# Kernel optimization log

Measured on AMD Instinct MI355X. Metric: run time of the kernel, lower is better.

## Reference

```python
import jax, jax.numpy as jnp
import numpy as np

EPS = 1e-5
POOL = 4  # two stacked AvgPool3d(2) == one AvgPool3d(4, stride=4) on the valid region


def setup_inputs() -> dict:
    key = jax.random.key(0)
    k1, k2, k3 = jax.random.split(key, 3)
    N, Cin, Cout, D = 16, 32, 16, 32
    x = jax.random.normal(k1, (N, Cin, D, D, D), dtype=jnp.float32)
    w = jax.random.normal(k2, (Cin, Cout, 3, 3, 3), dtype=jnp.float32) * 0.1
    b = jax.random.normal(k3, (Cout,), dtype=jnp.float32) * 0.1
    gamma = jnp.ones((Cout,), dtype=jnp.float32)
    beta = jnp.zeros((Cout,), dtype=jnp.float32)
    return {"x": x, "w": w, "b": b, "gamma": gamma, "beta": beta}


def _convT_bn_pool(x, w, b, gamma, beta):
    # ConvTranspose3d(stride=2, padding=1, K=3) == dilated conv with
    # lhs_dilation=2, padding=K-1-p=1, spatially-flipped kernel, IO->OI swap.
    wt = jnp.flip(w, axis=(2, 3, 4)).transpose(1, 0, 2, 3, 4)  # [Cout,Cin,3,3,3]
    y = jax.lax.conv_general_dilated(
        x, wt,
        window_strides=(1, 1, 1),
        padding=[(1, 1), (1, 1), (1, 1)],
        lhs_dilation=(2, 2, 2),
        dimension_numbers=("NCDHW", "OIDHW", "NCDHW"),
    )
    y = y + b[None, :, None, None, None]  # [N,Cout,Dout,Hout,Wout], Dout=2D-1

    # BatchNorm training stats: biased variance over (N,D,H,W) per channel
    mean = jnp.mean(y, axis=(0, 2, 3, 4), keepdims=True)
    var = jnp.mean(jnp.square(y - mean), axis=(0, 2, 3, 4), keepdims=True)
    inv = jax.lax.rsqrt(var + EPS)
    yn = (y - mean) * inv * gamma[None, :, None, None, None] + beta[None, :, None, None, None]

    # Two AvgPool3d(2) == AvgPool3d(4, stride 4) on the cropped valid region
    N_, C_, Do, Ho, Wo = yn.shape
    D2, H2, W2 = Do // POOL, Ho // POOL, Wo // POOL
    yn = yn[:, :, : D2 * POOL, : H2 * POOL, : W2 * POOL]
    yn = yn.reshape(N_, C_, D2, POOL, H2, POOL, W2, POOL)
    return jnp.mean(yn, axis=(3, 5, 7))  # [N,C,D2,H2,W2]


def reference(x, w, b, gamma, beta):
    return _convT_bn_pool(x, w, b, gamma, beta)
```

## Files before the change

kernel.cpp:

```cpp
#include <hip/hip_runtime.h>


typedef __attribute__((ext_vector_type(8))) short bf16x8;
typedef __attribute__((ext_vector_type(4))) float f32x4;
typedef __attribute__((ext_vector_type(2))) float f32x2;

static __device__ __forceinline__ unsigned short f2bf(float f) {
    unsigned int u = __float_as_uint(f);
    u = (u + 0x7fffu + ((u >> 16) & 1u)) >> 16;
    return (unsigned short)u;
}
static __device__ __forceinline__ unsigned cvtpk(float a, float b) {
    unsigned r;
    asm("v_cvt_pk_bf16_f32 %0, %1, %2" : "=v"(r) : "v"(a), "v"(b));
    return r;
}
static __device__ __forceinline__ void pkadd(f32x2& acc, f32x2 a) {
    asm("v_pk_add_f32 %0, %1, %0" : "+v"(acc) : "v"(a));
}
static __device__ __forceinline__ void pkfma(f32x2& acc, f32x2 a) {
    asm("v_pk_fma_f32 %0, %1, %1, %0" : "+v"(acc) : "v"(a));
}

__global__ __launch_bounds__(256)
void kw(const float* __restrict__ w, unsigned short* __restrict__ wT)
{
    const int idx = blockIdx.x * 256 + threadIdx.x;
    if (idx < 13824) {
        const int ci = idx & 31, co = (idx >> 5) & 15, tap = idx >> 9;
        const int s  = (ci >> 3) ^ ((co >> 1) & 3);
        const int dst = tap*512 + co*32 + s*8 + (ci & 7);
        wT[dst] = f2bf(w[(ci * 16 + co) * 27 + tap]);
    }
}

__global__ __launch_bounds__(512, 6)
void convf2(const float* __restrict__ x,
            const unsigned short* __restrict__ wT,
            const float* __restrict__ bias,
            float* __restrict__ pooled,
            float* __restrict__ psum, float* __restrict__ psq)
{
    const int ht = blockIdx.x, dt = blockIdx.y, n = blockIdx.z;
    const int tid = threadIdx.x;
    const int vv = tid >> 6, lane = tid & 63;
    const int tw = vv & 1, odq = vv >> 1;
    const int c = lane & 15, qd = lane >> 4;

    __shared__ alignas(16) unsigned short xs[9504];
    __shared__ alignas(16) unsigned short wTs[13824];
    __shared__ float sred[8][16], qred[8][16], pbuf[4][2][8][16];

    const float bv = bias[c];

    #pragma unroll
    for (int i = 0; i < 4; ++i) {
        const int chunk = vv + 8 * i;
        if (chunk < 27) {
            __builtin_amdgcn_global_load_lds(
                (const char*)wT + chunk * 1024 + lane * 16,
                (char*)wTs + chunk * 1024,
                16, 0, 0);
        }
    }

    const int h = tid >> 8, ltid = tid & 255;
    const int ciS = ltid >> 3, q = ltid & 7;
    const int oL = ciS & 7;
    const int g = ciS >> 3;
    const float* xbase = x + (size_t)(n*32 + ciS)*32768 + 4*q;
    float4 F[5];
    #pragma unroll
    for (int i = 0; i < 5; ++i) {
        const int p = 2*i + h;
        if (p < 9) {
            const int di = p / 3, hp = p - 3*(p/3);
            const int id = 2*dt + di, ih = 2*ht + hp;
            F[i] = (id < 32 && ih < 32)
                 ? *(const float4*)(xbase + id*1024 + ih*32)
                 : make_float4(0.f, 0.f, 0.f, 0.f);
        }
    }
    const unsigned selP = (lane & 8) ? 0x07060302u : 0x01000504u;
    const int iwT = 4*q + (oL & 3), hT = oL >> 2;
    #pragma unroll
    for (int i = 0; i < 5; ++i) {
        const int p = 2*i + h;
        if (p < 9) {
            unsigned u0 = cvtpk(F[i].x, F[i].y);
            unsigned u1 = cvtpk(F[i].z, F[i].w);
            const unsigned a0 = (unsigned)__shfl_xor((int)u0, 8, 64);
            const unsigned a1 = (unsigned)__shfl_xor((int)u1, 8, 64);
            u0 = __builtin_amdgcn_perm(u0, a0, selP);
            u1 = __builtin_amdgcn_perm(u1, a1, selP);
            const unsigned s0 = (unsigned)__shfl_xor((int)u0, 16, 64);
            const unsigned s1 = (unsigned)__shfl_xor((int)u1, 16, 64);
            const unsigned w0 = (lane & 16) ? s1 : u0;
            const unsigned w1 = (lane & 16) ? u1 : s0;
            *(uint2*)(xs + p*1056 + g*264 + iwT*8 + 4*hT) = make_uint2(w0, w1);
        }
    }
    if (tid < 36) {
        const int dihi = tid >> 2, gg = tid & 3;
        *(uint4*)(xs + dihi*1056 + gg*264 + 256) = make_uint4(0,0,0,0);
    }

    __syncthreads();

    f32x4 acc[4][2];
    #pragma unroll
    for (int oh = 0; oh < 4; ++oh)
        #pragma unroll
        for (int par = 0; par < 2; ++par)
            acc[oh][par] = (f32x4){0.f,0.f,0.f,0.f};

    const int iwb = 16 * tw + c;
    const unsigned short* Abase = xs + qd*264 + iwb*8;
    const unsigned short* Bbase = wTs + c*32 + (qd ^ ((c >> 1) & 3))*8;

    auto TRI = [&](int oh, const bf16x8& A0, const bf16x8& A1,
                   const bf16x8& B0, const bf16x8& B1, const bf16x8& B2) {
        acc[oh][0] = __builtin_amdgcn_mfma_f32_16x16x32_bf16(A0, B1, acc[oh][0], 0, 0, 0);
        acc[oh][1] = __builtin_amdgcn_mfma_f32_16x16x32_bf16(A1, B0, acc[oh][1], 0, 0, 0);
        acc[oh][1] = __builtin_amdgcn_mfma_f32_16x16x32_bf16(A0, B2, acc[oh][1], 0, 0, 0);
    };
    auto PH = [&](int tapbase, int di) {
        const unsigned short* Ab = Abase + di * 3168;
        bf16x8 Aa0 = *(const bf16x8*)(Ab + 0);
        bf16x8 Aa1 = *(const bf16x8*)(Ab + 8);
        bf16x8 Ab0 = *(const bf16x8*)(Ab + 1056);
        bf16x8 Ab1 = *(const bf16x8*)(Ab + 1056 + 8);
        {
            const bf16x8 B0 = *(const bf16x8*)(Bbase + (tapbase + 3)*512);
            const bf16x8 B1 = *(const bf16x8*)(Bbase + (tapbase + 4)*512);
            const bf16x8 B2 = *(const bf16x8*)(Bbase + (tapbase + 5)*512);
            TRI(0, Aa0, Aa1, B0, B1, B2);
            TRI(2, Ab0, Ab1, B0, B1, B2);
        }
        {
            const bf16x8 B0 = *(const bf16x8*)(Bbase + (tapbase + 6)*512);
            const bf16x8 B1 = *(const bf16x8*)(Bbase + (tapbase + 7)*512);
            const bf16x8 B2 = *(const bf16x8*)(Bbase + (tapbase + 8)*512);
            TRI(1, Aa0, Aa1, B0, B1, B2);
            TRI(3, Ab0, Ab1, B0, B1, B2);
        }
        {
            Aa0 = *(const bf16x8*)(Ab + 2112);
            Aa1 = *(const bf16x8*)(Ab + 2112 + 8);
            const bf16x8 B0 = *(const bf16x8*)(Bbase + (tapbase + 0)*512);
            const bf16x8 B1 = *(const bf16x8*)(Bbase + (tapbase + 1)*512);
            const bf16x8 B2 = *(const bf16x8*)(Bbase + (tapbase + 2)*512);
            TRI(1, Ab0, Ab1, B0, B1, B2);
            TRI(3, Aa0, Aa1, B0, B1, B2);
        }
    };
    const int m = odq >> 1;
    if ((odq & 1) == 0) {
        PH(9, m);
    } else {
        PH(18, m);
        PH(0,  m + 1);
    }

    const bool inter = (dt < 15) && (ht < 15);
    const bool owx = (tw == 1) && (qd == 3);
    float s_raw, sq_raw, cnt;
    float P0 = 0.f, P1 = 0.f;
    if (inter) {
        f32x2 Pa = (f32x2){0.f,0.f}, Pb = (f32x2){0.f,0.f};
        f32x2 Qa = (f32x2){0.f,0.f}, Qb = (f32x2){0.f,0.f};
        #pragma unroll
        for (int oh = 0; oh < 4; ++oh)
            #pragma unroll
            for (int par = 0; par < 2; ++par) {
                const f32x4 a = acc[oh][par];
                const f32x2 lo = (f32x2){a[0], a[1]};
                const f32x2 hi = (f32x2){a[2], a[3]};
                pkadd(Pa, lo); pkfma(Qa, lo);
                pkadd(Pb, hi); pkfma(Qb, hi);
            }
        P0 = Pa[0] + Pa[1];
        P1 = Pb[0] + Pb[1];
        float sqr = (Qa[0] + Qa[1]) + (Qb[0] + Qb[1]);
        float corr = 0.f, corrq = 0.f;
        if (owx) {
            #pragma unroll
            for (int oh = 0; oh < 4; ++oh) {
                const float a = acc[oh][1][3];
                corr += a; corrq = fmaf(a, a, corrq);
            }
        }
        s_raw  = (P0 + P1) - corr;
        sq_raw = sqr - corrq;
        cnt    = owx ? 28.f : 32.f;
    } else {
        s_raw = 0.f; sq_raw = 0.f; cnt = 0.f;
        const bool odok = !(dt == 15 && odq == 3);
        #pragma unroll
        for (int oh = 0; oh < 4; ++oh) {
            const bool ohok = !(ht == 15 && oh == 3);
            #pragma unroll
            for (int par = 0; par < 2; ++par)
                #pragma unroll
                for (int r = 0; r < 4; ++r) {
                    const float a = acc[oh][par][r];
                    const bool owok = !(par == 1 && owx && r == 3);
                    const float mk = (odok && ohok && owok) ? 1.f : 0.f;
                    const float t = mk * a;
                    s_raw += t; sq_raw = fmaf(t, a, sq_raw); cnt += mk;
                    P0 += (r < 2) ? t : 0.f;
                    P1 += (r >= 2) ? t : 0.f;
                }
        }
    }
    float s_b  = fmaf(cnt, bv, s_raw);
    float sq_b = fmaf(fmaf(cnt, bv, 2.f * s_raw), bv, sq_raw);

    s_b  += __shfl_xor(s_b, 16, 64);  s_b  += __shfl_xor(s_b, 32, 64);
    sq_b += __shfl_xor(sq_b, 16, 64); sq_b += __shfl_xor(sq_b, 32, 64);
    if (lane < 16) { sred[vv][lane] = s_b; qred[vv][lane] = sq_b; }
    pbuf[odq][tw][2*qd + 0][c] = P0;
    pbuf[odq][tw][2*qd + 1][c] = P1;

    __syncthreads();

    if (tid < 16) {
        const int blk = (n*16 + dt)*16 + ht;
        float S = 0.f, Q = 0.f;
        #pragma unroll
        for (int wv = 0; wv < 8; ++wv) { S += sred[wv][tid]; Q += qred[wv][tid]; }
        psum[tid*4096 + blk] = S;
        psq [tid*4096 + blk] = Q;
    }
    if (odq == 3 && inter) {
        #pragma unroll
        for (int jj = 0; jj < 2; ++jj) {
            const int jl = 2*qd + jj, jg = 8*tw + jl;
            if (jg < 15) {
                const float tot = pbuf[0][tw][jl][c] + pbuf[1][tw][jl][c]
                                + pbuf[2][tw][jl][c] + pbuf[3][tw][jl][c];
                pooled[(n*16 + c)*3375 + dt*225 + ht*15 + jg] = tot * (1.f/64.f);
            }
        }
    }
}

__global__ void bnfinal(const float* __restrict__ psum, const float* __restrict__ psq,
                        const float* __restrict__ gamma, const float* __restrict__ beta,
                        const float* __restrict__ bias,
                        float* __restrict__ bn)
{
    const int co = blockIdx.x;
    const int t  = threadIdx.x;
    float S = 0, Q = 0;
    for (int blk = t; blk < 4096; blk += 256) {
        S += psum[co*4096 + blk];
        Q += psq [co*4096 + blk];
    }
    #pragma unroll
    for (int off = 32; off > 0; off >>= 1) {
        S += __shfl_down(S, off, 64);
        Q += __shfl_down(Q, off, 64);
    }
    __shared__ float rs[4], rq[4];
    if ((t & 63) == 0) { rs[t >> 6] = S; rq[t >> 6] = Q; }
    __syncthreads();
    if (t == 0) {
        S = rs[0] + rs[1] + rs[2] + rs[3];
        Q = rq[0] + rq[1] + rq[2] + rq[3];
        const float cnt = 16.f * 63.f * 63.f * 63.f;
        const float mean = S / cnt;
        const float var  = Q / cnt - mean * mean;
        const float inv  = rsqrtf(var + 1e-5f);
        const float sc   = inv * gamma[co];
        bn[co]      = sc;
        bn[16 + co] = beta[co] + (bias[co] - mean) * sc;
    }
}

__global__ void finalize(const float* __restrict__ pooled, const float* __restrict__ bn,
                         float* __restrict__ out)
{
    const int i  = blockIdx.x * 256 + threadIdx.x;
    const int co = (i / 3375) & 15;
    out[i] = pooled[i] * bn[co] + bn[16 + co];
}

extern "C" void kernel_launch(void* const* d_in, const int* in_sizes, int n_in,
                              void* d_out, int out_size, void* d_ws, size_t ws_size,
                              hipStream_t stream)
{
    const float* x     = (const float*)d_in[0];
    const float* w     = (const float*)d_in[1];
    const float* b     = (const float*)d_in[2];
    const float* gamma = (const float*)d_in[3];
    const float* beta  = (const float*)d_in[4];
    float* out = (float*)d_out;

    char* wsb = (char*)d_ws;
    unsigned short* wT = (unsigned short*)wsb;
    float* pooled = (float*)(wsb + 27648);
    float* psum   = (float*)(wsb + 27648 + 3456000);
    float* psq    = (float*)(wsb + 27648 + 3456000 + 262144);
    float* bn     = (float*)(wsb + 27648 + 3456000 + 2*262144);

    kw<<<54, 256, 0, stream>>>(w, wT);
    dim3 grid(16, 16, 16);
    convf2<<<grid, 512, 0, stream>>>(x, wT, b, pooled, psum, psq);
    bnfinal<<<16, 256, 0, stream>>>(psum, psq, gamma, beta, b, bn);
    finalize<<<3375, 256, 0, stream>>>(pooled, bn, out);
}
```

Measured before the change: 128.7 us.

## Loop each conv block over 8 batch items with double-buffered input staging

Each conv block now handles 8 batch samples instead of one, cutting the grid from 4096 to 512 blocks. The weight tile is loaded into LDS once per block and reused across the 8 samples. Global loads for the next sample are issued before the current sample's MFMAs, and the transposed tile goes into a second LDS buffer to overlap memory with compute. The cost is 512 blocks on a large GPU, possibly leaving CUs idle, plus extra LDS use and more syncs per block; the launch bound drops to 4 blocks per CU.

New measurement: 122.6 us. 1.05x faster.

```diff
diff --git a/kernel.cpp b/kernel.cpp
--- a/kernel.cpp
+++ b/kernel.cpp
@@ -34,20 +34,21 @@
     }
 }
 
-__global__ __launch_bounds__(512, 6)
+__global__ __launch_bounds__(512, 4)
 void convf2(const float* __restrict__ x,
             const unsigned short* __restrict__ wT,
             const float* __restrict__ bias,
             float* __restrict__ pooled,
             float* __restrict__ psum, float* __restrict__ psq)
 {
-    const int ht = blockIdx.x, dt = blockIdx.y, n = blockIdx.z;
+    const int ht = blockIdx.x, dt = blockIdx.y, bz = blockIdx.z;
+    const int n0 = bz * 8;
     const int tid = threadIdx.x;
     const int vv = tid >> 6, lane = tid & 63;
     const int tw = vv & 1, odq = vv >> 1;
     const int c = lane & 15, qd = lane >> 4;
 
-    __shared__ alignas(16) unsigned short xs[9504];
+    __shared__ alignas(16) unsigned short xs[2][9504];
     __shared__ alignas(16) unsigned short wTs[13824];
     __shared__ float sred[8][16], qred[8][16], pbuf[4][2][8][16];
 
@@ -68,133 +69,194 @@
     const int ciS = ltid >> 3, q = ltid & 7;
     const int oL = ciS & 7;
     const int g = ciS >> 3;
-    const float* xbase = x + (size_t)(n*32 + ciS)*32768 + 4*q;
-    float4 F[5];
+    int offp[5]; bool okp[5];
     #pragma unroll
     for (int i = 0; i < 5; ++i) {
         const int p = 2*i + h;
-        if (p < 9) {
-            const int di = p / 3, hp = p - 3*(p/3);
-            const int id = 2*dt + di, ih = 2*ht + hp;
-            F[i] = (id < 32 && ih < 32)
-                 ? *(const float4*)(xbase + id*1024 + ih*32)
-                 : make_float4(0.f, 0.f, 0.f, 0.f);
-        }
-    }
+        const int di = p / 3, hp = p - 3*(p/3);
+        const int id = 2*dt + di, ih = 2*ht + hp;
+        okp[i]  = (p < 9) && (id < 32) && (ih < 32);
+        offp[i] = id*1024 + ih*32;
+    }
+    const float* xci = x + (size_t)ciS*32768 + 4*q;
+    float4 F[5];
+    auto ISSUE = [&](int nn) {
+        const float* xb = xci + (size_t)nn*32*32768;
+        #pragma unroll
+        for (int i = 0; i < 5; ++i)
+            F[i] = okp[i] ? *(const float4*)(xb + offp[i])
+                          : make_float4(0.f, 0.f, 0.f, 0.f);
+    };
     const unsigned selP = (lane & 8) ? 0x07060302u : 0x01000504u;
     const int iwT = 4*q + (oL & 3), hT = oL >> 2;
-    #pragma unroll
-    for (int i = 0; i < 5; ++i) {
-        const int p = 2*i + h;
-        if (p < 9) {
-            unsigned u0 = cvtpk(F[i].x, F[i].y);
-            unsigned u1 = cvtpk(F[i].z, F[i].w);
-            const unsigned a0 = (unsigned)__shfl_xor((int)u0, 8, 64);
-            const unsigned a1 = (unsigned)__shfl_xor((int)u1, 8, 64);
-            u0 = __builtin_amdgcn_perm(u0, a0, selP);
-            u1 = __builtin_amdgcn_perm(u1, a1, selP);
-            const unsigned s0 = (unsigned)__shfl_xor((int)u0, 16, 64);
-            const unsigned s1 = (unsigned)__shfl_xor((int)u1, 16, 64);
-            const unsigned w0 = (lane & 16) ? s1 : u0;
-            const unsigned w1 = (lane & 16) ? u1 : s0;
-            *(uint2*)(xs + p*1056 + g*264 + iwT*8 + 4*hT) = make_uint2(w0, w1);
-        }
-    }
+    auto TRANSP = [&](unsigned short* xp) {
+        #pragma unroll
+        for (int i = 0; i < 5; ++i) {
+            const int p = 2*i + h;
+            if (p < 9) {
+                unsigned u0 = cvtpk(F[i].x, F[i].y);
+                unsigned u1 = cvtpk(F[i].z, F[i].w);
+                const unsigned a0 = (unsigned)__shfl_xor((int)u0, 8, 64);
+                const unsigned a1 = (unsigned)__shfl_xor((int)u1, 8, 64);
+                u0 = __builtin_amdgcn_perm(u0, a0, selP);
+                u1 = __builtin_amdgcn_perm(u1, a1, selP);
+                const unsigned s0 = (unsigned)__shfl_xor((int)u0, 16, 64);
+                const unsigned s1 = (unsigned)__shfl_xor((int)u1, 16, 64);
+                const unsigned w0 = (lane & 16) ? s1 : u0;
+                const unsigned w1 = (lane & 16) ? u1 : s0;
+                *(uint2*)(xp + p*1056 + g*264 + iwT*8 + 4*hT) = make_uint2(w0, w1);
+            }
+        }
+    };
+
+    ISSUE(n0);
     if (tid < 36) {
         const int dihi = tid >> 2, gg = tid & 3;
-        *(uint4*)(xs + dihi*1056 + gg*264 + 256) = make_uint4(0,0,0,0);
-    }
-
+        *(uint4*)(&xs[0][0] + dihi*1056 + gg*264 + 256) = make_uint4(0,0,0,0);
+        *(uint4*)(&xs[1][0] + dihi*1056 + gg*264 + 256) = make_uint4(0,0,0,0);
+    }
+    TRANSP(&xs[0][0]);
     __syncthreads();
 
-    f32x4 acc[4][2];
-    #pragma unroll
-    for (int oh = 0; oh < 4; ++oh)
-        #pragma unroll
-        for (int par = 0; par < 2; ++par)
-            acc[oh][par] = (f32x4){0.f,0.f,0.f,0.f};
-
     const int iwb = 16 * tw + c;
-    const unsigned short* Abase = xs + qd*264 + iwb*8;
     const unsigned short* Bbase = wTs + c*32 + (qd ^ ((c >> 1) & 3))*8;
-
-    auto TRI = [&](int oh, const bf16x8& A0, const bf16x8& A1,
-                   const bf16x8& B0, const bf16x8& B1, const bf16x8& B2) {
-        acc[oh][0] = __builtin_amdgcn_mfma_f32_16x16x32_bf16(A0, B1, acc[oh][0], 0, 0, 0);
-        acc[oh][1] = __builtin_amdgcn_mfma_f32_16x16x32_bf16(A1, B0, acc[oh][1], 0, 0, 0);
-        acc[oh][1] = __builtin_amdgcn_mfma_f32_16x16x32_bf16(A0, B2, acc[oh][1], 0, 0, 0);
-    };
-    auto PH = [&](int tapbase, int di) {
-        const unsigned short* Ab = Abase + di * 3168;
-        bf16x8 Aa0 = *(const bf16x8*)(Ab + 0);
-        bf16x8 Aa1 = *(const bf16x8*)(Ab + 8);
-        bf16x8 Ab0 = *(const bf16x8*)(Ab + 1056);
-        bf16x8 Ab1 = *(const bf16x8*)(Ab + 1056 + 8);
-        {
-            const bf16x8 B0 = *(const bf16x8*)(Bbase + (tapbase + 3)*512);
-            const bf16x8 B1 = *(const bf16x8*)(Bbase + (tapbase + 4)*512);
-            const bf16x8 B2 = *(const bf16x8*)(Bbase + (tapbase + 5)*512);
-            TRI(0, Aa0, Aa1, B0, B1, B2);
-            TRI(2, Ab0, Ab1, B0, B1, B2);
-        }
-        {
-            const bf16x8 B0 = *(const bf16x8*)(Bbase + (tapbase + 6)*512);
-            const bf16x8 B1 = *(const bf16x8*)(Bbase + (tapbase + 7)*512);
-            const bf16x8 B2 = *(const bf16x8*)(Bbase + (tapbase + 8)*512);
-            TRI(1, Aa0, Aa1, B0, B1, B2);
-            TRI(3, Ab0, Ab1, B0, B1, B2);
-        }
-        {
-            Aa0 = *(const bf16x8*)(Ab + 2112);
-            Aa1 = *(const bf16x8*)(Ab + 2112 + 8);
-            const bf16x8 B0 = *(const bf16x8*)(Bbase + (tapbase + 0)*512);
-            const bf16x8 B1 = *(const bf16x8*)(Bbase + (tapbase + 1)*512);
-            const bf16x8 B2 = *(const bf16x8*)(Bbase + (tapbase + 2)*512);
-            TRI(1, Ab0, Ab1, B0, B1, B2);
-            TRI(3, Aa0, Aa1, B0, B1, B2);
-        }
-    };
-    const int m = odq >> 1;
-    if ((odq & 1) == 0) {
-        PH(9, m);
-    } else {
-        PH(18, m);
-        PH(0,  m + 1);
-    }
-
     const bool inter = (dt < 15) && (ht < 15);
     const bool owx = (tw == 1) && (qd == 3);
-    float s_raw, sq_raw, cnt;
-    float P0 = 0.f, P1 = 0.f;
+    const int m = odq >> 1;
+
+    float s_rawA = 0.f, sq_rawA = 0.f;
+
+    for (int tt = 0; tt < 8; ++tt) {
+        const int cur = tt & 1;
+        if (tt < 7) ISSUE(n0 + tt + 1);
+
+        f32x4 acc[4][2];
+        #pragma unroll
+        for (int oh = 0; oh < 4; ++oh)
+            #pragma unroll
+            for (int par = 0; par < 2; ++par)
+                acc[oh][par] = (f32x4){0.f,0.f,0.f,0.f};
+
+        const unsigned short* Abase = &xs[cur][0] + qd*264 + iwb*8;
+
+        auto TRI = [&](int oh, const bf16x8& A0, const bf16x8& A1,
+                       const bf16x8& B0, const bf16x8& B1, const bf16x8& B2) {
+            acc[oh][0] = __builtin_amdgcn_mfma_f32_16x16x32_bf16(A0, B1, acc[oh][0], 0, 0, 0);
+            acc[oh][1] = __builtin_amdgcn_mfma_f32_16x16x32_bf16(A1, B0, acc[oh][1], 0, 0, 0);
+            acc[oh][1] = __builtin_amdgcn_mfma_f32_16x16x32_bf16(A0, B2, acc[oh][1], 0, 0, 0);
+        };
+        auto PH = [&](int tapbase, int di) {
+            const unsigned short* Ab = Abase + di * 3168;
+            bf16x8 Aa0 = *(const bf16x8*)(Ab + 0);
+            bf16x8 Aa1 = *(const bf16x8*)(Ab + 8);
+            bf16x8 Ab0 = *(const bf16x8*)(Ab + 1056);
+            bf16x8 Ab1 = *(const bf16x8*)(Ab + 1056 + 8);
+            {
+                const bf16x8 B0 = *(const bf16x8*)(Bbase + (tapbase + 3)*512);
+                const bf16x8 B1 = *(const bf16x8*)(Bbase + (tapbase + 4)*512);
+                const bf16x8 B2 = *(const bf16x8*)(Bbase + (tapbase + 5)*512);
+                TRI(0, Aa0, Aa1, B0, B1, B2);
+                TRI(2, Ab0, Ab1, B0, B1, B2);
+            }
+            {
+                const bf16x8 B0 = *(const bf16x8*)(Bbase + (tapbase + 6)*512);
+                const bf16x8 B1 = *(const bf16x8*)(Bbase + (tapbase + 7)*512);
+                const bf16x8 B2 = *(const bf16x8*)(Bbase + (tapbase + 8)*512);
+                TRI(1, Aa0, Aa1, B0, B1, B2);
+                TRI(3, Ab0, Ab1, B0, B1, B2);
+            }
+            {
+                Aa0 = *(const bf16x8*)(Ab + 2112);
+                Aa1 = *(const bf16x8*)(Ab + 2112 + 8);
+                const bf16x8 B0 = *(const bf16x8*)(Bbase + (tapbase + 0)*512);
+                const bf16x8 B1 = *(const bf16x8*)(Bbase + (tapbase + 1)*512);
+                const bf16x8 B2 = *(const bf16x8*)(Bbase + (tapbase + 2)*512);
+                TRI(1, Ab0, Ab1, B0, B1, B2);
+                TRI(3, Aa0, Aa1, B0, B1, B2);
+            }
+        };
+        if ((odq & 1) == 0) {
+            PH(9, m);
+        } else {
+            PH(18, m);
+            PH(0,  m + 1);
+        }
+
+        float s_raw, sq_raw;
+        float P0 = 0.f, P1 = 0.f;
+        if (inter) {
+            f32x2 Pa = (f32x2){0.f,0.f}, Pb = (f32x2){0.f,0.f};
+            f32x2 Qa = (f32x2){0.f,0.f}, Qb = (f32x2){0.f,0.f};
+            #pragma unroll
+            for (int oh = 0; oh < 4; ++oh)
+                #pragma unroll
+                for (int par = 0; par < 2; ++par) {
+                    const f32x4 a = acc[oh][par];
+                    const f32x2 lo = (f32x2){a[0], a[1]};
+                    const f32x2 hi = (f32x2){a[2], a[3]};
+                    pkadd(Pa, lo); pkfma(Qa, lo);
+                    pkadd(Pb, hi); pkfma(Qb, hi);
+                }
+            P0 = Pa[0] + Pa[1];
+            P1 = Pb[0] + Pb[1];
+            float sqr = (Qa[0] + Qa[1]) + (Qb[0] + Qb[1]);
+            float corr = 0.f, corrq = 0.f;
+            if (owx) {
+                #pragma unroll
+                for (int oh = 0; oh < 4; ++oh) {
+                    const float a = acc[oh][1][3];
+                    corr += a; corrq = fmaf(a, a, corrq);
+                }
+            }
+            s_raw  = (P0 + P1) - corr;
+            sq_raw = sqr - corrq;
+        } else {
+            s_raw = 0.f; sq_raw = 0.f;
+            const bool odok = !(dt == 15 && odq == 3);
+            #pragma unroll
+            for (int oh = 0; oh < 4; ++oh) {
+                const bool ohok = !(ht == 15 && oh == 3);
+                #pragma unroll
+                for (int par = 0; par < 2; ++par)
+                    #pragma unroll
+                    for (int r = 0; r < 4; ++r) {
+                        const float a = acc[oh][par][r];
+                        const bool owok = !(par == 1 && owx && r == 3);
+                        const float mk = (odok && ohok && owok) ? 1.f : 0.f;
+                        const float t = mk * a;
+                        s_raw += t; sq_raw = fmaf(t, a, sq_raw);
+                    }
+            }
+        }
+        s_rawA += s_raw; sq_rawA += sq_raw;
+
+        pbuf[odq][tw][2*qd + 0][c] = P0;
+        pbuf[odq][tw][2*qd + 1][c] = P1;
+        __syncthreads();
+
+        if (odq == 3 && inter) {
+            #pragma unroll
+            for (int jj = 0; jj < 2; ++jj) {
+                const int jl = 2*qd + jj, jg = 8*tw + jl;
+                if (jg < 15) {
+                    const float tot = pbuf[0][tw][jl][c] + pbuf[1][tw][jl][c]
+                                    + pbuf[2][tw][jl][c] + pbuf[3][tw][jl][c];
+                    pooled[((n0 + tt)*16 + c)*3375 + dt*225 + ht*15 + jg]
+                        = tot * (1.f/64.f);
+                }
+            }
+        }
+        if (tt < 7) {
+            TRANSP(&xs[cur ^ 1][0]);
+            __syncthreads();
+        }
+    }
+
+    float cnt1;
     if (inter) {
-        f32x2 Pa = (f32x2){0.f,0.f}, Pb = (f32x2){0.f,0.f};
-        f32x2 Qa = (f32x2){0.f,0.f}, Qb = (f32x2){0.f,0.f};
-        #pragma unroll
-        for (int oh = 0; oh < 4; ++oh)
-            #pragma unroll
-            for (int par = 0; par < 2; ++par) {
-                const f32x4 a = acc[oh][par];
-                const f32x2 lo = (f32x2){a[0], a[1]};
-                const f32x2 hi = (f32x2){a[2], a[3]};
-                pkadd(Pa, lo); pkfma(Qa, lo);
-                pkadd(Pb, hi); pkfma(Qb, hi);
-            }
-        P0 = Pa[0] + Pa[1];
-        P1 = Pb[0] + Pb[1];
-        float sqr = (Qa[0] + Qa[1]) + (Qb[0] + Qb[1]);
-        float corr = 0.f, corrq = 0.f;
-        if (owx) {
-            #pragma unroll
-            for (int oh = 0; oh < 4; ++oh) {
-                const float a = acc[oh][1][3];
-                corr += a; corrq = fmaf(a, a, corrq);
-            }
-        }
-        s_raw  = (P0 + P1) - corr;
-        sq_raw = sqr - corrq;
-        cnt    = owx ? 28.f : 32.f;
+        cnt1 = owx ? 28.f : 32.f;
     } else {
-        s_raw = 0.f; sq_raw = 0.f; cnt = 0.f;
+        cnt1 = 0.f;
         const bool odok = !(dt == 15 && odq == 3);
         #pragma unroll
         for (int oh = 0; oh < 4; ++oh) {
@@ -203,45 +265,27 @@
             for (int par = 0; par < 2; ++par)
                 #pragma unroll
                 for (int r = 0; r < 4; ++r) {
-                    const float a = acc[oh][par][r];
                     const bool owok = !(par == 1 && owx && r == 3);
-                    const float mk = (odok && ohok && owok) ? 1.f : 0.f;
-                    const float t = mk * a;
-                    s_raw += t; sq_raw = fmaf(t, a, sq_raw); cnt += mk;
-                    P0 += (r < 2) ? t : 0.f;
-                    P1 += (r >= 2) ? t : 0.f;
+                    cnt1 += (odok && ohok && owok) ? 1.f : 0.f;
                 }
         }
     }
-    float s_b  = fmaf(cnt, bv, s_raw);
-    float sq_b = fmaf(fmaf(cnt, bv, 2.f * s_raw), bv, sq_raw);
+    const float cnt8 = 8.f * cnt1;
+    float s_b  = fmaf(cnt8, bv, s_rawA);
+    float sq_b = fmaf(fmaf(cnt8, bv, 2.f * s_rawA), bv, sq_rawA);
 
     s_b  += __shfl_xor(s_b, 16, 64);  s_b  += __shfl_xor(s_b, 32, 64);
     sq_b += __shfl_xor(sq_b, 16, 64); sq_b += __shfl_xor(sq_b, 32, 64);
     if (lane < 16) { sred[vv][lane] = s_b; qred[vv][lane] = sq_b; }
-    pbuf[odq][tw][2*qd + 0][c] = P0;
-    pbuf[odq][tw][2*qd + 1][c] = P1;
-
     __syncthreads();
 
     if (tid < 16) {
-        const int blk = (n*16 + dt)*16 + ht;
+        const int blk = (bz*16 + dt)*16 + ht;
         float S = 0.f, Q = 0.f;
         #pragma unroll
         for (int wv = 0; wv < 8; ++wv) { S += sred[wv][tid]; Q += qred[wv][tid]; }
-        psum[tid*4096 + blk] = S;
-        psq [tid*4096 + blk] = Q;
-    }
-    if (odq == 3 && inter) {
-        #pragma unroll
-        for (int jj = 0; jj < 2; ++jj) {
-            const int jl = 2*qd + jj, jg = 8*tw + jl;
-            if (jg < 15) {
-                const float tot = pbuf[0][tw][jl][c] + pbuf[1][tw][jl][c]
-                                + pbuf[2][tw][jl][c] + pbuf[3][tw][jl][c];
-                pooled[(n*16 + c)*3375 + dt*225 + ht*15 + jg] = tot * (1.f/64.f);
-            }
-        }
+        psum[tid*512 + blk] = S;
+        psq [tid*512 + blk] = Q;
     }
 }
 
@@ -253,9 +297,9 @@
     const int co = blockIdx.x;
     const int t  = threadIdx.x;
     float S = 0, Q = 0;
-    for (int blk = t; blk < 4096; blk += 256) {
-        S += psum[co*4096 + blk];
-        Q += psq [co*4096 + blk];
+    for (int blk = t; blk < 512; blk += 256) {
+        S += psum[co*512 + blk];
+        Q += psq [co*512 + blk];
     }
     #pragma unroll
     for (int off = 32; off > 0; off >>= 1) {
@@ -305,7 +349,7 @@
     float* bn     = (float*)(wsb + 27648 + 3456000 + 2*262144);
 
     kw<<<54, 256, 0, stream>>>(w, wT);
-    dim3 grid(16, 16, 16);
+    dim3 grid(16, 16, 2);
     convf2<<<grid, 512, 0, stream>>>(x, wT, b, pooled, psum, psq);
     bnfinal<<<16, 256, 0, stream>>>(psum, psq, gamma, beta, b, bn);
     finalize<<<3375, 256, 0, stream>>>(pooled, bn, out);
```
